# Optimization experiments

Measured on AMD Instinct MI355X. Metric: run time of the kernel, lower is better.

Reference implementation:

```python
import jax, jax.numpy as jnp
import numpy as np

N_NODES = 100000
N_EDGES = 600000
D = 128


def gcn_conv(x, W, b, src, dst, n_nodes):
    """PyG-style GCNConv: add self-loops, symmetric deg^{-1/2} normalization."""
    xw = x @ W  # [N, out]
    # degree of destination nodes, counting the added self-loop
    deg = jnp.zeros((n_nodes,), xw.dtype).at[dst].add(1.0) + 1.0
    dinv = jax.lax.rsqrt(deg)
    coef = dinv[src] * dinv[dst]  # [E]
    agg = jnp.zeros_like(xw).at[dst].add(xw[src] * coef[:, None])
    agg = agg + xw * (dinv * dinv)[:, None]  # self-loop term
    return agg + b


def setup_inputs() -> dict:
    key = jax.random.key(0)
    k = jax.random.split(key, 9)
    s = 1.0 / np.sqrt(D)
    return {
        "x": jax.random.normal(k[0], (N_NODES, D), jnp.float32),
        "edge_index_pos": jax.random.randint(k[1], (2, N_EDGES), 0, N_NODES, jnp.int64),
        "edge_index_neg": jax.random.randint(k[2], (2, N_EDGES), 0, N_NODES, jnp.int64),
        "W1": jax.random.uniform(k[3], (D, D), jnp.float32, -s, s),
        "b1": jnp.zeros((D,), jnp.float32),
        "W2": jax.random.uniform(k[4], (D, D), jnp.float32, -s, s),
        "b2": jnp.zeros((D,), jnp.float32),
        "weight": jax.random.uniform(k[5], (2 * D, D), jnp.float32, -s, s),
        "bias": jnp.zeros((D,), jnp.float32),
    }


def reference(x, edge_index_pos, edge_index_neg, W1, b1, W2, b2, weight, bias):
    n = x.shape[0]
    h1 = gcn_conv(x, W1, b1, edge_index_pos[0], edge_index_pos[1], n)  # [N, D]
    h2 = gcn_conv(x, W2, b2, edge_index_neg[0], edge_index_neg[1], n)  # [N, D]
    h = jnp.concatenate([h1, h2], axis=-1)  # [N, 2D]
    return h @ weight + bias  # [N, D]
```

## Files before the change

### kernel.cpp

```cpp
#include <hip/hip_runtime.h>

#define N_NODES 100000
#define NT (2 * N_NODES)
#define D 128
#define N_EDGES 600000
#define ET (2 * N_EDGES)
#define SCAN_B 256
#define NBLK2 ((NT + SCAN_B - 1) / SCAN_B)
#define FBLK ((N_NODES + 127) / 128)
#define ZBLK ((NT / 4 + 255) / 256)

typedef __attribute__((ext_vector_type(8))) short bf16x8;
typedef __attribute__((ext_vector_type(4))) float f32x4;

__device__ __forceinline__ unsigned short f2bf(float f) {
    union { float f; unsigned u; } v; v.f = f;
    unsigned r = (v.u + 0x7fff + ((v.u >> 16) & 1)) >> 16;
    return (unsigned short)r;
}
__device__ __forceinline__ float bf2f(unsigned short h) {
    union { unsigned u; float f; } v; v.u = ((unsigned)h) << 16;
    return v.f;
}

__device__ __forceinline__ long long load_idx(const void* e, long long i, int is32) {
    if (is32) return (long long)((const int*)e)[i];
    return ((const long long*)e)[i];
}

__global__ void prep_all(const float* __restrict__ W1, const float* __restrict__ W2,
                         const float* __restrict__ weight,
                         const float* __restrict__ b1, const float* __restrict__ b2,
                         const float* __restrict__ bias,
                         const unsigned long long* __restrict__ e_pos,
                         unsigned short* __restrict__ Mt, float* __restrict__ bt,
                         int* __restrict__ flag, int* __restrict__ degi) {
    if (blockIdx.x < 128) {
        int idx = blockIdx.x * 256 + threadIdx.x;
        int j = idx >> 8, k = idx & 255;
        float a = 0.f;
        if (k < D) {
            for (int d = 0; d < D; ++d) a += W1[k * D + d] * weight[d * D + j];
        } else {
            for (int d = 0; d < D; ++d) a += W2[(k - D) * D + d] * weight[(D + d) * D + j];
        }
        Mt[j * 256 + k] = f2bf(a);
    } else if (blockIdx.x == 128) {
        int t = threadIdx.x;
        if (t < D) {
            float a = bias[t];
            for (int k = 0; k < D; ++k)
                a += b1[k] * weight[k * D + t] + b2[k] * weight[(D + k) * D + t];
            bt[t] = a;
        } else if (t < 192) {
            unsigned long long v = e_pos[t - 128];
            unsigned long long m = __ballot(v > 0xFFFFFFFFull);
            if (t == 128) *flag = (m != 0ull) ? 1 : 0;
        }
    } else {
        int i = (blockIdx.x - 129) * 256 + threadIdx.x;
        if (i < NT / 4) ((int4*)degi)[i] = make_int4(0, 0, 0, 0);
    }
}

__global__ void x2bf_degree(const float* __restrict__ x, unsigned short* __restrict__ xb,
                            const void* __restrict__ ep, const void* __restrict__ en,
                            const int* __restrict__ flag, int* __restrict__ degi) {
    if (blockIdx.x < 12500) {
        long long t = (long long)blockIdx.x * 256 + threadIdx.x;
        float4 a = ((const float4*)x)[t];
        ((ushort4*)xb)[t] = make_ushort4(f2bf(a.x), f2bf(a.y), f2bf(a.z), f2bf(a.w));
    } else {
        int i = (blockIdx.x - 12500) * 256 + threadIdx.x;
        if (i >= ET) return;
        int is32 = *flag;
        int conv = (i >= N_EDGES);
        const void* e = conv ? en : ep;
        int j = conv ? i - N_EDGES : i;
        long long d = load_idx(e, (long long)N_EDGES + j, is32);
        atomicAdd(&degi[conv * N_NODES + (int)d], 1);
    }
}

__global__ void scan_pass1(const int* __restrict__ degi, int* __restrict__ bsum,
                           float* __restrict__ dinv) {
    __shared__ int sm[SCAN_B];
    int i = blockIdx.x * SCAN_B + threadIdx.x;
    int v = (i < NT) ? degi[i] : 0;
    if (i < NT) dinv[i] = rsqrtf((float)v + 1.0f);
    sm[threadIdx.x] = v;
    __syncthreads();
    for (int s = SCAN_B / 2; s > 0; s >>= 1) {
        if (threadIdx.x < s) sm[threadIdx.x] += sm[threadIdx.x + s];
        __syncthreads();
    }
    if (threadIdx.x == 0) bsum[blockIdx.x] = sm[0];
}

__global__ void scan_pass3(const int* __restrict__ degi, const int* __restrict__ bsum,
                           int* __restrict__ off) {
    __shared__ int red[SCAN_B];
    __shared__ int sm[SCAN_B];
    int partial = 0;
    for (int i = threadIdx.x; i < blockIdx.x; i += SCAN_B) partial += bsum[i];
    red[threadIdx.x] = partial;
    __syncthreads();
    for (int s = SCAN_B / 2; s > 0; s >>= 1) {
        if (threadIdx.x < s) red[threadIdx.x] += red[threadIdx.x + s];
        __syncthreads();
    }
    int base = red[0];
    int i = blockIdx.x * SCAN_B + threadIdx.x;
    int v = (i < NT) ? degi[i] : 0;
    sm[threadIdx.x] = v;
    __syncthreads();
    for (int ofs = 1; ofs < SCAN_B; ofs <<= 1) {
        int add = (threadIdx.x >= ofs) ? sm[threadIdx.x - ofs] : 0;
        __syncthreads();
        sm[threadIdx.x] += add;
        __syncthreads();
    }
    int excl = sm[threadIdx.x] - v + base;
    if (i < NT) off[i] = excl;
    if (i == NT - 1) off[NT] = excl + v;
}

__global__ void csr_fill_both(const void* __restrict__ ep, const void* __restrict__ en,
                              const int* __restrict__ flag, const int* __restrict__ off,
                              int* __restrict__ degi, const float* __restrict__ dinv,
                              int2* __restrict__ csr) {
    int i = blockIdx.x * blockDim.x + threadIdx.x;
    if (i >= ET) return;
    int is32 = *flag;
    int conv = (i >= N_EDGES);
    const void* e = conv ? en : ep;
    int j = conv ? i - N_EDGES : i;
    int si = (int)load_idx(e, j, is32);
    int di = (int)load_idx(e, (long long)N_EDGES + j, is32);
    int g = conv * N_NODES;
    int node = g + di;
    int pos = off[node] + atomicSub(&degi[node], 1) - 1;
    float coef = dinv[g + si] * dinv[node];
    csr[pos] = make_int2(si, __float_as_int(coef));
}

__global__ __launch_bounds__(512) void fused_gather_gemm(
    const int* __restrict__ off, const int2* __restrict__ csr,
    const unsigned short* __restrict__ xb, const float* __restrict__ dinv,
    const unsigned short* __restrict__ Mt, const float* __restrict__ bt,
    float* __restrict__ out) {
    __shared__ unsigned short mlds[128][264];
    int t = threadIdx.x;
    for (int c = t; c < 4096; c += 512) {
        int row = c >> 5;
        int kc = (c & 31) * 8;
        *(ulonglong2*)&mlds[row][kc] = *(const ulonglong2*)&Mt[row * 256 + kc];
    }
    __syncthreads();

    int wave = t >> 6, lane = t & 63;
    int rl = lane & 15, q = lane >> 4;
    int gr = blockIdx.x * 128 + wave * 16 + rl;
    const bool valid = gr < N_NODES;

    bf16x8 af[8];
    #pragma unroll
    for (int conv = 0; conv < 2; ++conv) {
        float acc[4][8];
        if (valid) {
            int n = conv * N_NODES + gr;
            float dn = dinv[n];
            float f = dn * dn;
            const unsigned short* xr = xb + (size_t)gr * D + q * 8;
            #pragma unroll
            for (int m = 0; m < 4; ++m) {
                bf16x8 v = *(const bf16x8*)(xr + m * 32);
                #pragma unroll
                for (int j = 0; j < 8; ++j) acc[m][j] = bf2f((unsigned short)v[j]) * f;
            }
            int e0 = off[n], e1 = off[n + 1];
            for (int e = e0; e < e1; ++e) {
                int2 sc = csr[e];
                float coef = __int_as_float(sc.y);
                const unsigned short* xs = xb + (size_t)sc.x * D + q * 8;
                #pragma unroll
                for (int m = 0; m < 4; ++m) {
                    bf16x8 v = *(const bf16x8*)(xs + m * 32);
                    #pragma unroll
                    for (int j = 0; j < 8; ++j) acc[m][j] += coef * bf2f((unsigned short)v[j]);
                }
            }
        } else {
            #pragma unroll
            for (int m = 0; m < 4; ++m)
                #pragma unroll
                for (int j = 0; j < 8; ++j) acc[m][j] = 0.f;
        }
        #pragma unroll
        for (int m = 0; m < 4; ++m) {
            bf16x8 a;
            #pragma unroll
            for (int j = 0; j < 8; ++j) a[j] = (short)f2bf(acc[m][j]);
            af[conv * 4 + m] = a;
        }
    }

    f32x4 C[8];
    #pragma unroll
    for (int i = 0; i < 8; ++i) C[i] = (f32x4){0.f, 0.f, 0.f, 0.f};
    #pragma unroll
    for (int ks = 0; ks < 8; ++ks) {
        bf16x8 afr = af[ks];
        #pragma unroll
        for (int ct = 0; ct < 8; ++ct) {
            bf16x8 bfr = *(const bf16x8*)&mlds[ct * 16 + rl][ks * 32 + q * 8];
            C[ct] = __builtin_amdgcn_mfma_f32_16x16x32_bf16(afr, bfr, C[ct], 0, 0, 0);
        }
    }

    int orow = blockIdx.x * 128 + wave * 16 + q * 4;
    #pragma unroll
    for (int ct = 0; ct < 8; ++ct) {
        int col = ct * 16 + rl;
        float b = bt[col];
        #pragma unroll
        for (int reg = 0; reg < 4; ++reg) {
            int row = orow + reg;
            if (row < N_NODES) out[(long long)row * D + col] = C[ct][reg] + b;
        }
    }
}

extern "C" void kernel_launch(void* const* d_in, const int* in_sizes, int n_in,
                              void* d_out, int out_size, void* d_ws, size_t ws_size,
                              hipStream_t stream) {
    const float* x      = (const float*)d_in[0];
    const void*  e_pos  = d_in[1];
    const void*  e_neg  = d_in[2];
    const float* W1     = (const float*)d_in[3];
    const float* b1     = (const float*)d_in[4];
    const float* W2     = (const float*)d_in[5];
    const float* b2     = (const float*)d_in[6];
    const float* weight = (const float*)d_in[7];
    const float* bias   = (const float*)d_in[8];
    float* out = (float*)d_out;

    unsigned short* xb = (unsigned short*)d_ws;
    unsigned short* Mt = xb + (size_t)N_NODES * D;
    float* bt   = (float*)(Mt + 128 * 256);
    float* dinv = bt + D;
    int*   flag = (int*)(dinv + NT);
    int*   degi = flag + 4;
    int*   off  = degi + NT;
    int*   bsum = off + NT + 4;
    int2*  csr  = (int2*)(bsum + 1024);

    prep_all<<<129 + ZBLK, 256, 0, stream>>>(W1, W2, weight, b1, b2, bias,
                                             (const unsigned long long*)e_pos,
                                             Mt, bt, flag, degi);
    const int egrid = (ET + 255) / 256;
    x2bf_degree<<<12500 + egrid, 256, 0, stream>>>(x, xb, e_pos, e_neg, flag, degi);
    scan_pass1<<<NBLK2, SCAN_B, 0, stream>>>(degi, bsum, dinv);
    scan_pass3<<<NBLK2, SCAN_B, 0, stream>>>(degi, bsum, off);
    csr_fill_both<<<egrid, 256, 0, stream>>>(e_pos, e_neg, flag, off, degi, dinv, csr);
    fused_gather_gemm<<<FBLK, 512, 0, stream>>>(off, csr, xb, dinv, Mt, bt, out);
}
```

Baseline: 222.9 us.

## Pack CSR entries into 32 bits and enlarge gather-GEMM blocks

Each CSR entry shrinks from an int2 (source index plus precomputed coefficient) to one 32-bit word. The word holds a 20-bit source index and the source degree clamped to 8 bits, and the gather loop recomputes the coefficient with rsqrt. This halves CSR storage and read traffic, at the cost of an rsqrt per edge, and gives wrong normalisation for any node with degree above 255. Separately, the fused gather-GEMM kernel now launches 1024 threads covering 256 rows per block. That spreads the weight load into LDS over more rows but tightens the per-thread register budget, which could cause spills.

```diff
diff --git a/kernel.cpp b/kernel.cpp
--- a/kernel.cpp
+++ b/kernel.cpp
@@ -7,7 +7,8 @@
 #define ET (2 * N_EDGES)
 #define SCAN_B 256
 #define NBLK2 ((NT + SCAN_B - 1) / SCAN_B)
-#define FBLK ((N_NODES + 127) / 128)
+#define FROWS 256
+#define FBLK ((N_NODES + FROWS - 1) / FROWS)
 #define ZBLK ((NT / 4 + 255) / 256)
 
 typedef __attribute__((ext_vector_type(8))) short bf16x8;
@@ -83,11 +84,14 @@
 }
 
 __global__ void scan_pass1(const int* __restrict__ degi, int* __restrict__ bsum,
-                           float* __restrict__ dinv) {
+                           float* __restrict__ dinv, unsigned char* __restrict__ degb) {
     __shared__ int sm[SCAN_B];
     int i = blockIdx.x * SCAN_B + threadIdx.x;
     int v = (i < NT) ? degi[i] : 0;
-    if (i < NT) dinv[i] = rsqrtf((float)v + 1.0f);
+    if (i < NT) {
+        dinv[i] = rsqrtf((float)v + 1.0f);
+        degb[i] = (unsigned char)(v > 255 ? 255 : v);
+    }
     sm[threadIdx.x] = v;
     __syncthreads();
     for (int s = SCAN_B / 2; s > 0; s >>= 1) {
@@ -127,8 +131,8 @@
 
 __global__ void csr_fill_both(const void* __restrict__ ep, const void* __restrict__ en,
                               const int* __restrict__ flag, const int* __restrict__ off,
-                              int* __restrict__ degi, const float* __restrict__ dinv,
-                              int2* __restrict__ csr) {
+                              int* __restrict__ degi, const unsigned char* __restrict__ degb,
+                              unsigned* __restrict__ csr) {
     int i = blockIdx.x * blockDim.x + threadIdx.x;
     if (i >= ET) return;
     int is32 = *flag;
@@ -140,18 +144,18 @@
     int g = conv * N_NODES;
     int node = g + di;
     int pos = off[node] + atomicSub(&degi[node], 1) - 1;
-    float coef = dinv[g + si] * dinv[node];
-    csr[pos] = make_int2(si, __float_as_int(coef));
-}
-
-__global__ __launch_bounds__(512) void fused_gather_gemm(
-    const int* __restrict__ off, const int2* __restrict__ csr,
+    unsigned degS = degb[g + si];
+    csr[pos] = (unsigned)si | (degS << 20);
+}
+
+__global__ __launch_bounds__(1024) void fused_gather_gemm(
+    const int* __restrict__ off, const unsigned* __restrict__ csr,
     const unsigned short* __restrict__ xb, const float* __restrict__ dinv,
     const unsigned short* __restrict__ Mt, const float* __restrict__ bt,
     float* __restrict__ out) {
     __shared__ unsigned short mlds[128][264];
     int t = threadIdx.x;
-    for (int c = t; c < 4096; c += 512) {
+    for (int c = t; c < 4096; c += 1024) {
         int row = c >> 5;
         int kc = (c & 31) * 8;
         *(ulonglong2*)&mlds[row][kc] = *(const ulonglong2*)&Mt[row * 256 + kc];
@@ -160,7 +164,7 @@
 
     int wave = t >> 6, lane = t & 63;
     int rl = lane & 15, q = lane >> 4;
-    int gr = blockIdx.x * 128 + wave * 16 + rl;
+    int gr = blockIdx.x * FROWS + wave * 16 + rl;
     const bool valid = gr < N_NODES;
 
     bf16x8 af[8];
@@ -180,9 +184,10 @@
             }
             int e0 = off[n], e1 = off[n + 1];
             for (int e = e0; e < e1; ++e) {
-                int2 sc = csr[e];
-                float coef = __int_as_float(sc.y);
-                const unsigned short* xs = xb + (size_t)sc.x * D + q * 8;
+                unsigned sc = csr[e];
+                int si = sc & 0xFFFFF;
+                float coef = dn * rsqrtf((float)(sc >> 20) + 1.0f);
+                const unsigned short* xs = xb + (size_t)si * D + q * 8;
                 #pragma unroll
                 for (int m = 0; m < 4; ++m) {
                     bf16x8 v = *(const bf16x8*)(xs + m * 32);
@@ -218,7 +223,7 @@
         }
     }
 
-    int orow = blockIdx.x * 128 + wave * 16 + q * 4;
+    int orow = blockIdx.x * FROWS + wave * 16 + q * 4;
     #pragma unroll
     for (int ct = 0; ct < 8; ++ct) {
         int col = ct * 16 + rl;
@@ -253,15 +258,16 @@
     int*   degi = flag + 4;
     int*   off  = degi + NT;
     int*   bsum = off + NT + 4;
-    int2*  csr  = (int2*)(bsum + 1024);
+    unsigned char* degb = (unsigned char*)(bsum + 1024);
+    unsigned* csr = (unsigned*)(degb + NT);
 
     prep_all<<<129 + ZBLK, 256, 0, stream>>>(W1, W2, weight, b1, b2, bias,
                                              (const unsigned long long*)e_pos,
                                              Mt, bt, flag, degi);
     const int egrid = (ET + 255) / 256;
     x2bf_degree<<<12500 + egrid, 256, 0, stream>>>(x, xb, e_pos, e_neg, flag, degi);
-    scan_pass1<<<NBLK2, SCAN_B, 0, stream>>>(degi, bsum, dinv);
+    scan_pass1<<<NBLK2, SCAN_B, 0, stream>>>(degi, bsum, dinv, degb);
     scan_pass3<<<NBLK2, SCAN_B, 0, stream>>>(degi, bsum, off);
-    csr_fill_both<<<egrid, 256, 0, stream>>>(e_pos, e_neg, flag, off, degi, dinv, csr);
-    fused_gather_gemm<<<FBLK, 512, 0, stream>>>(off, csr, xb, dinv, Mt, bt, out);
-}
+    csr_fill_both<<<egrid, 256, 0, stream>>>(e_pos, e_neg, flag, off, degi, degb, csr);
+    fused_gather_gemm<<<FBLK, 1024, 0, stream>>>(off, csr, xb, dinv, Mt, bt, out);
+}
```

Result: no change. 224.0 us (+0.5%).
